# Performance work log

Measured on AMD Instinct MI355X. Metric: run time of the kernel, lower is better.

The kernel has to match this reference:

```python
import jax, jax.numpy as jnp
import numpy as np

N_NODES = 100000
N_EDGES = 1600000
IN_FEATS = 128
OUT_FEATS = 32


def setup_inputs() -> dict:
    key = jax.random.key(0)
    k1, k2, k3, k4 = jax.random.split(key, 4)
    inputs = jax.random.normal(k1, (N_NODES, IN_FEATS), dtype=jnp.float32)
    weight = jax.random.normal(k2, (IN_FEATS, OUT_FEATS), dtype=jnp.float32)
    src = jax.random.randint(k3, (N_EDGES,), 0, N_NODES, dtype=jnp.int32)
    dst = jax.random.randint(k4, (N_EDGES,), 0, N_NODES, dtype=jnp.int32)
    return {"inputs": inputs, "weight": weight, "src": src, "dst": dst}


def reference(inputs, weight, src, dst):
    # GCNLayer.forward: dense projection then sparse sum-aggregation (gspmmv,
    # no normalization: norm flags False/False -> plain neighbor sum).
    h = inputs @ weight                      # [N, out_feats]
    msgs = h[src]                            # gather over edges [E, out_feats]
    out = jax.ops.segment_sum(msgs, dst, num_segments=inputs.shape[0])
    return out
```

## Files before the change

kernel.cpp:

```cpp
#include <hip/hip_runtime.h>
#include <hip/hip_bf16.h>

#define N_F_IN 128
#define N_F_OUT 32

#define BSHIFT 7
#define BNODES 128
#define BCAP 2560
#define SCAT_EDGES 4096
#define NBL 1024
#define OFFT_LD 400

typedef __attribute__((ext_vector_type(8))) short short8v;
typedef __attribute__((ext_vector_type(4))) float float4v;

static __device__ __forceinline__ unsigned bf16pair(float a, float b) {
    unsigned ua = __float_as_uint(a), ub = __float_as_uint(b);
    ua = (ua + 0x7FFFu + ((ua >> 16) & 1u)) >> 16;
    ub = (ub + 0x7FFFu + ((ub >> 16) & 1u)) >> 16;
    return ua | (ub << 16);
}
static __device__ __forceinline__ unsigned short bf16r(float a) {
    unsigned ua = __float_as_uint(a);
    return (unsigned short)((ua + 0x7FFFu + ((ua >> 16) & 1u)) >> 16);
}

union SharedU {
    unsigned short wT[32 * 136];
    struct {
        int A[NBL];
        int B[NBL];
        int wsum[8];
        int lrec[SCAT_EDGES];
    } sc;
};

__global__ __launch_bounds__(512, 8) void fused2_kernel(const float* __restrict__ x,
                                                        const float* __restrict__ w,
                                                        unsigned short* __restrict__ hb,
                                                        int n,
                                                        const int* __restrict__ src,
                                                        const int* __restrict__ dst,
                                                        int* __restrict__ recs,
                                                        unsigned short* __restrict__ offT,
                                                        int E) {
    __shared__ SharedU u;
    const int t = threadIdx.x;
    const int nch = (E + SCAT_EDGES - 1) / SCAT_EDGES;
    const int chunk = blockIdx.x >> 1;

    if (((blockIdx.x & 1) == 0) && (chunk < nch)) {
        const int e0 = chunk * SCAT_EDGES;
        const int cnt = min(SCAT_EDGES, E - e0);

        int dv[8], sv[8];
        #pragma unroll
        for (int j = 0; j < 8; ++j) {
            int i = t + j * 512;
            dv[j] = -1; sv[j] = 0;
            if (i < cnt) { dv[j] = dst[e0 + i]; sv[j] = src[e0 + i]; }
        }

        for (int i = t; i < NBL; i += 512) u.sc.A[i] = 0;
        __syncthreads();

        #pragma unroll
        for (int j = 0; j < 8; ++j)
            if (dv[j] >= 0) atomicAdd(&u.sc.A[dv[j] >> BSHIFT], 1);
        __syncthreads();

        const int b0 = t * 2;
        const int c0 = u.sc.A[b0], c1 = u.sc.A[b0 + 1];
        const int tot = c0 + c1;
        const int lane = t & 63;
        const int wv8 = t >> 6;
        int sc = tot;
        #pragma unroll
        for (int off = 1; off < 64; off <<= 1) {
            int v = __shfl_up(sc, off, 64);
            if (lane >= off) sc += v;
        }
        if (lane == 63) u.sc.wsum[wv8] = sc;
        __syncthreads();
        int wbase = 0;
        #pragma unroll
        for (int ww = 0; ww < 7; ++ww) wbase += (ww < wv8) ? u.sc.wsum[ww] : 0;
        const int base = wbase + sc - tot;
        u.sc.B[b0] = base;
        u.sc.B[b0 + 1] = base + c0;
        offT[(long)b0 * OFFT_LD + chunk]       = (unsigned short)base;
        offT[(long)(b0 + 1) * OFFT_LD + chunk] = (unsigned short)(base + c0);
        __syncthreads();

        #pragma unroll
        for (int j = 0; j < 8; ++j) {
            if (dv[j] >= 0) {
                int r = atomicAdd(&u.sc.B[dv[j] >> BSHIFT], 1);
                u.sc.lrec[r] = ((dv[j] & (BNODES - 1)) << 17) | sv[j];
            }
        }
        __syncthreads();

        {
            int* rp = recs + (long)chunk * SCAT_EDGES;
            for (int i = t; i < cnt; i += 512) rp[i] = u.sc.lrec[i];
        }
        __syncthreads();
    }

    {
        const float4* w4 = (const float4*)w;
        float4 a = w4[t * 2], bq = w4[t * 2 + 1];
        int idx = t * 8;
        u.wT[((idx + 0) & 31) * 136 + ((idx + 0) >> 5)] = bf16r(a.x);
        u.wT[((idx + 1) & 31) * 136 + ((idx + 1) >> 5)] = bf16r(a.y);
        u.wT[((idx + 2) & 31) * 136 + ((idx + 2) >> 5)] = bf16r(a.z);
        u.wT[((idx + 3) & 31) * 136 + ((idx + 3) >> 5)] = bf16r(a.w);
        u.wT[((idx + 4) & 31) * 136 + ((idx + 4) >> 5)] = bf16r(bq.x);
        u.wT[((idx + 5) & 31) * 136 + ((idx + 5) >> 5)] = bf16r(bq.y);
        u.wT[((idx + 6) & 31) * 136 + ((idx + 6) >> 5)] = bf16r(bq.z);
        u.wT[((idx + 7) & 31) * 136 + ((idx + 7) >> 5)] = bf16r(bq.w);
    }
    __syncthreads();

    const int wv = t >> 6;
    const int l = t & 63;
    const int lr = l & 15;
    const int lg = l >> 4;

    const int ntiles = (n + 15) >> 4;
    const int mtile = blockIdx.x * 8 + wv;
    if (mtile < ntiles) {
        const long R0 = (long)mtile * 16;
        long rr = R0 + lr; if (rr >= n) rr = n - 1;
        const float4* q = (const float4*)(x + rr * N_F_IN) + lg * 2;

        const unsigned short* wr0 = &u.wT[lr * 136];
        const unsigned short* wr1 = &u.wT[(16 + lr) * 136];

        float4 p0 = q[0], p1 = q[1], p2 = q[8], p3 = q[9];
        float4v acc0 = {0.f, 0.f, 0.f, 0.f}, acc1 = {0.f, 0.f, 0.f, 0.f};
        #pragma unroll
        for (int ks = 0; ks < 4; ++ks) {
            float4 lo, hi;
            if (ks & 1) { lo = p2; hi = p3; } else { lo = p0; hi = p1; }
            union { short8v v; unsigned uu[4]; } af;
            af.uu[0] = bf16pair(lo.x, lo.y);
            af.uu[1] = bf16pair(lo.z, lo.w);
            af.uu[2] = bf16pair(hi.x, hi.y);
            af.uu[3] = bf16pair(hi.z, hi.w);
            if (ks == 0) { p0 = q[16]; p1 = q[17]; }
            if (ks == 1) { p2 = q[24]; p3 = q[25]; }
            short8v bf0 = *(const short8v*)(wr0 + ks * 32 + lg * 8);
            short8v bf1 = *(const short8v*)(wr1 + ks * 32 + lg * 8);
            acc0 = __builtin_amdgcn_mfma_f32_16x16x32_bf16(af.v, bf0, acc0, 0, 0, 0);
            acc1 = __builtin_amdgcn_mfma_f32_16x16x32_bf16(af.v, bf1, acc1, 0, 0, 0);
        }
        #pragma unroll
        for (int reg = 0; reg < 4; ++reg) {
            long row = R0 + lg * 4 + reg;
            if (row < n) {
                hb[row * N_F_OUT + lr]      = bf16r(acc0[reg]);
                hb[row * N_F_OUT + 16 + lr] = bf16r(acc1[reg]);
            }
        }
    }
}

__global__ __launch_bounds__(512) void agg_kernel(const unsigned short* __restrict__ hb,
                                                  const unsigned short* __restrict__ offT,
                                                  const int* __restrict__ recs,
                                                  float* __restrict__ out, int n, int nch) {
    __shared__ unsigned short s_st[OFFT_LD], s_en[OFFT_LD];
    __shared__ int dof[512];
    __shared__ int srt0[BCAP];
    __shared__ int srt[BCAP];
    __shared__ int cN[BNODES], loff[BNODES + 1], lc[BNODES], wsum8[8];
    __shared__ int s_tot;
    const int t = threadIdx.x;
    const int b = blockIdx.x;

    for (int i = t; i < nch; i += 512) {
        s_st[i] = offT[(long)b * OFFT_LD + i];
        s_en[i] = offT[(long)(b + 1) * OFFT_LD + i];
    }
    if (t < BNODES) cN[t] = 0;
    __syncthreads();

    const int cc = (t < nch) ? ((int)s_en[t] - (int)s_st[t]) : 0;
    const int lane = t & 63;
    const int wv = t >> 6;
    int sc = cc;
    #pragma unroll
    for (int off = 1; off < 64; off <<= 1) {
        int v = __shfl_up(sc, off, 64);
        if (lane >= off) sc += v;
    }
    if (lane == 63) wsum8[wv] = sc;
    __syncthreads();
    int wbase = 0;
    #pragma unroll
    for (int ww = 0; ww < 7; ++ww) wbase += (ww < wv) ? wsum8[ww] : 0;
    dof[t] = wbase + sc - cc;
    if (t == 511) s_tot = wbase + sc;
    __syncthreads();
    const int cnt = min(s_tot, BCAP);

    for (int i = t; i < cnt; i += 512) {
        int lo = 0, hi = nch;
        while (hi - lo > 1) {
            int mid = (lo + hi) >> 1;
            if (dof[mid] <= i) lo = mid; else hi = mid;
        }
        srt0[i] = recs[(long)lo * SCAT_EDGES + (int)s_st[lo] + (i - dof[lo])];
    }
    __syncthreads();

    int i = t;
    for (; i + 1536 < cnt; i += 2048) {
        int r0 = srt0[i],        r1 = srt0[i + 512];
        int r2 = srt0[i + 1024], r3 = srt0[i + 1536];
        atomicAdd(&cN[(r0 >> 17) & (BNODES - 1)], 1);
        atomicAdd(&cN[(r1 >> 17) & (BNODES - 1)], 1);
        atomicAdd(&cN[(r2 >> 17) & (BNODES - 1)], 1);
        atomicAdd(&cN[(r3 >> 17) & (BNODES - 1)], 1);
    }
    for (; i < cnt; i += 512)
        atomicAdd(&cN[(srt0[i] >> 17) & (BNODES - 1)], 1);
    __syncthreads();

    if (t < 64) {
        int v0 = cN[2 * t], v1 = cN[2 * t + 1];
        int s = v0 + v1;
        #pragma unroll
        for (int off = 1; off < 64; off <<= 1) {
            int v = __shfl_up(s, off, 64);
            if (t >= off) s += v;
        }
        int ex = s - v0 - v1;
        loff[2 * t] = ex;
        loff[2 * t + 1] = ex + v0;
        lc[2 * t] = ex;
        lc[2 * t + 1] = ex + v0;
        if (t == 63) loff[BNODES] = s;
    }
    __syncthreads();

    i = t;
    for (; i + 1536 < cnt; i += 2048) {
        int r0 = srt0[i],        r1 = srt0[i + 512];
        int r2 = srt0[i + 1024], r3 = srt0[i + 1536];
        int k0 = atomicAdd(&lc[(r0 >> 17) & (BNODES - 1)], 1); srt[k0] = r0 & 0x1FFFF;
        int k1 = atomicAdd(&lc[(r1 >> 17) & (BNODES - 1)], 1); srt[k1] = r1 & 0x1FFFF;
        int k2 = atomicAdd(&lc[(r2 >> 17) & (BNODES - 1)], 1); srt[k2] = r2 & 0x1FFFF;
        int k3 = atomicAdd(&lc[(r3 >> 17) & (BNODES - 1)], 1); srt[k3] = r3 & 0x1FFFF;
    }
    for (; i < cnt; i += 512) {
        int r0 = srt0[i];
        int k0 = atomicAdd(&lc[(r0 >> 17) & (BNODES - 1)], 1); srt[k0] = r0 & 0x1FFFF;
    }
    __syncthreads();

    const uint2* hq = (const uint2*)hb;
    #pragma unroll
    for (int pp = 0; pp < 2; ++pp) {
        int nl = pp * 64 + (t >> 3);
        int jj = t & 7;
        int beg = loff[nl], end = loff[nl + 1];
        float4 a0 = make_float4(0.f, 0.f, 0.f, 0.f);
        float4 a1 = a0, a2 = a0, a3 = a0;
        int k = beg;
        for (; k + 4 <= end; k += 4) {
            uint2 v0 = hq[(size_t)srt[k] * 8 + jj];
            uint2 v1 = hq[(size_t)srt[k + 1] * 8 + jj];
            uint2 v2 = hq[(size_t)srt[k + 2] * 8 + jj];
            uint2 v3 = hq[(size_t)srt[k + 3] * 8 + jj];
            a0.x += __uint_as_float(v0.x << 16); a0.y += __uint_as_float(v0.x & 0xFFFF0000u);
            a0.z += __uint_as_float(v0.y << 16); a0.w += __uint_as_float(v0.y & 0xFFFF0000u);
            a1.x += __uint_as_float(v1.x << 16); a1.y += __uint_as_float(v1.x & 0xFFFF0000u);
            a1.z += __uint_as_float(v1.y << 16); a1.w += __uint_as_float(v1.y & 0xFFFF0000u);
            a2.x += __uint_as_float(v2.x << 16); a2.y += __uint_as_float(v2.x & 0xFFFF0000u);
            a2.z += __uint_as_float(v2.y << 16); a2.w += __uint_as_float(v2.y & 0xFFFF0000u);
            a3.x += __uint_as_float(v3.x << 16); a3.y += __uint_as_float(v3.x & 0xFFFF0000u);
            a3.z += __uint_as_float(v3.y << 16); a3.w += __uint_as_float(v3.y & 0xFFFF0000u);
        }
        for (; k < end; ++k) {
            uint2 v0 = hq[(size_t)srt[k] * 8 + jj];
            a0.x += __uint_as_float(v0.x << 16); a0.y += __uint_as_float(v0.x & 0xFFFF0000u);
            a0.z += __uint_as_float(v0.y << 16); a0.w += __uint_as_float(v0.y & 0xFFFF0000u);
        }
        float4 a = make_float4(a0.x + a1.x + a2.x + a3.x, a0.y + a1.y + a2.y + a3.y,
                               a0.z + a1.z + a2.z + a3.z, a0.w + a1.w + a2.w + a3.w);
        long node = (long)b * BNODES + nl;
        if (node < n) *(float4*)&out[node * N_F_OUT + jj * 4] = a;
    }
}

extern "C" void kernel_launch(void* const* d_in, const int* in_sizes, int n_in,
                              void* d_out, int out_size, void* d_ws, size_t ws_size,
                              hipStream_t stream) {
    const float* x = (const float*)d_in[0];
    const float* w = (const float*)d_in[1];
    const int* src = (const int*)d_in[2];
    const int* dst = (const int*)d_in[3];
    float* out = (float*)d_out;

    const int n = in_sizes[0] / N_F_IN;
    const int E = in_sizes[2];
    const int NB = (n + BNODES - 1) >> BSHIFT;
    const int nch = (E + SCAT_EDGES - 1) / SCAT_EDGES;

    char* p = (char*)d_ws;
    unsigned short* hb = (unsigned short*)p;
    p += (((size_t)n * N_F_OUT * sizeof(unsigned short)) + 255) & ~(size_t)255;
    int* recs = (int*)p;
    p += (((size_t)nch * SCAT_EDGES * sizeof(int)) + 255) & ~(size_t)255;
    unsigned short* offT = (unsigned short*)p;
    p += (((size_t)1025 * OFFT_LD * sizeof(unsigned short)) + 255) & ~(size_t)255;

    const int ntiles = (n + 15) >> 4;
    int nblk = (ntiles + 7) >> 3;
    if (nblk < 2 * nch) nblk = 2 * nch;

    fused2_kernel<<<nblk, 512, 0, stream>>>(x, w, hb, n, src, dst, recs, offT, E);
    agg_kernel<<<NB, 512, 0, stream>>>(hb, offT, recs, out, n, nch);
}
```

Measured before the change: 56.58 us.

## Rebalance GEMM tiles across scatter/GEMM block pairs and replace binary search in aggregation

In the fused kernel, each block pair now shares 16 GEMM tiles: the scatter block takes 5 and the GEMM-only block takes 11, so work is balanced against the scatter cost. The weight load is hoisted ahead of the scatter phase, and the record copy-out is vectorized to int4. In the aggregation kernel, the per-element binary search over chunk offsets is replaced by a marker array plus a max prefix scan, with the bucket counting fused into the gather. The gather loop is unrolled to 8 loads with two accumulators. These changes add a few more barriers and more register pressure.

```diff
diff --git a/kernel.cpp b/kernel.cpp
--- a/kernel.cpp
+++ b/kernel.cpp
@@ -47,10 +47,14 @@
     __shared__ SharedU u;
     const int t = threadIdx.x;
     const int nch = (E + SCAT_EDGES - 1) / SCAT_EDGES;
-    const int chunk = blockIdx.x >> 1;
-
-    if (((blockIdx.x & 1) == 0) && (chunk < nch)) {
-        const int e0 = chunk * SCAT_EDGES;
+    const int pair = blockIdx.x >> 1;
+    const bool isScat = ((blockIdx.x & 1) == 0) && (pair < nch);
+
+    const float4* w4 = (const float4*)w;
+    const float4 wa = w4[t * 2], wb = w4[t * 2 + 1];
+
+    if (isScat) {
+        const int e0 = pair * SCAT_EDGES;
         const int cnt = min(SCAT_EDGES, E - e0);
 
         int dv[8], sv[8];
@@ -88,8 +92,8 @@
         const int base = wbase + sc - tot;
         u.sc.B[b0] = base;
         u.sc.B[b0 + 1] = base + c0;
-        offT[(long)b0 * OFFT_LD + chunk]       = (unsigned short)base;
-        offT[(long)(b0 + 1) * OFFT_LD + chunk] = (unsigned short)(base + c0);
+        offT[(long)b0 * OFFT_LD + pair]       = (unsigned short)base;
+        offT[(long)(b0 + 1) * OFFT_LD + pair] = (unsigned short)(base + c0);
         __syncthreads();
 
         #pragma unroll
@@ -102,41 +106,42 @@
         __syncthreads();
 
         {
-            int* rp = recs + (long)chunk * SCAT_EDGES;
-            for (int i = t; i < cnt; i += 512) rp[i] = u.sc.lrec[i];
+            int* rp = recs + (long)pair * SCAT_EDGES;
+            const int4* lr4 = (const int4*)u.sc.lrec;
+            int4* rp4 = (int4*)rp;
+            const int c4 = cnt >> 2;
+            for (int i = t; i < c4; i += 512) rp4[i] = lr4[i];
+            for (int i = (c4 << 2) + t; i < cnt; i += 512) rp[i] = u.sc.lrec[i];
         }
         __syncthreads();
     }
 
     {
-        const float4* w4 = (const float4*)w;
-        float4 a = w4[t * 2], bq = w4[t * 2 + 1];
         int idx = t * 8;
-        u.wT[((idx + 0) & 31) * 136 + ((idx + 0) >> 5)] = bf16r(a.x);
-        u.wT[((idx + 1) & 31) * 136 + ((idx + 1) >> 5)] = bf16r(a.y);
-        u.wT[((idx + 2) & 31) * 136 + ((idx + 2) >> 5)] = bf16r(a.z);
-        u.wT[((idx + 3) & 31) * 136 + ((idx + 3) >> 5)] = bf16r(a.w);
-        u.wT[((idx + 4) & 31) * 136 + ((idx + 4) >> 5)] = bf16r(bq.x);
-        u.wT[((idx + 5) & 31) * 136 + ((idx + 5) >> 5)] = bf16r(bq.y);
-        u.wT[((idx + 6) & 31) * 136 + ((idx + 6) >> 5)] = bf16r(bq.z);
-        u.wT[((idx + 7) & 31) * 136 + ((idx + 7) >> 5)] = bf16r(bq.w);
-    }
-    __syncthreads();
-
-    const int wv = t >> 6;
+        u.wT[((idx + 0) & 31) * 136 + ((idx + 0) >> 5)] = bf16r(wa.x);
+        u.wT[((idx + 1) & 31) * 136 + ((idx + 1) >> 5)] = bf16r(wa.y);
+        u.wT[((idx + 2) & 31) * 136 + ((idx + 2) >> 5)] = bf16r(wa.z);
+        u.wT[((idx + 3) & 31) * 136 + ((idx + 3) >> 5)] = bf16r(wa.w);
+        u.wT[((idx + 4) & 31) * 136 + ((idx + 4) >> 5)] = bf16r(wb.x);
+        u.wT[((idx + 5) & 31) * 136 + ((idx + 5) >> 5)] = bf16r(wb.y);
+        u.wT[((idx + 6) & 31) * 136 + ((idx + 6) >> 5)] = bf16r(wb.z);
+        u.wT[((idx + 7) & 31) * 136 + ((idx + 7) >> 5)] = bf16r(wb.w);
+    }
+    __syncthreads();
+
+    const int wvid = t >> 6;
     const int l = t & 63;
     const int lr = l & 15;
     const int lg = l >> 4;
-
     const int ntiles = (n + 15) >> 4;
-    const int mtile = blockIdx.x * 8 + wv;
-    if (mtile < ntiles) {
+
+    const unsigned short* wr0 = &u.wT[lr * 136];
+    const unsigned short* wr1 = &u.wT[(16 + lr) * 136];
+
+    auto gemm_tile = [&](int mtile) {
         const long R0 = (long)mtile * 16;
         long rr = R0 + lr; if (rr >= n) rr = n - 1;
         const float4* q = (const float4*)(x + rr * N_F_IN) + lg * 2;
-
-        const unsigned short* wr0 = &u.wT[lr * 136];
-        const unsigned short* wr1 = &u.wT[(16 + lr) * 136];
 
         float4 p0 = q[0], p1 = q[1], p2 = q[8], p3 = q[9];
         float4v acc0 = {0.f, 0.f, 0.f, 0.f}, acc1 = {0.f, 0.f, 0.f, 0.f};
@@ -164,6 +169,17 @@
                 hb[row * N_F_OUT + 16 + lr] = bf16r(acc1[reg]);
             }
         }
+    };
+
+    const int tbase = pair * 16;
+    if (blockIdx.x & 1) {
+        int m0 = tbase + 5 + wvid;
+        if (m0 < ntiles) gemm_tile(m0);
+        int m1 = tbase + 13 + wvid;
+        if (wvid < 3 && m1 < ntiles) gemm_tile(m1);
+    } else {
+        int m0 = tbase + wvid;
+        if (wvid < 5 && m0 < ntiles) gemm_tile(m0);
     }
 }
 
@@ -171,25 +187,23 @@
                                                   const unsigned short* __restrict__ offT,
                                                   const int* __restrict__ recs,
                                                   float* __restrict__ out, int n, int nch) {
-    __shared__ unsigned short s_st[OFFT_LD], s_en[OFFT_LD];
+    __shared__ unsigned short s_st[OFFT_LD];
     __shared__ int dof[512];
     __shared__ int srt0[BCAP];
-    __shared__ int srt[BCAP];
+    __shared__ int chk_srt[BCAP];
     __shared__ int cN[BNODES], loff[BNODES + 1], lc[BNODES], wsum8[8];
     __shared__ int s_tot;
     const int t = threadIdx.x;
     const int b = blockIdx.x;
-
-    for (int i = t; i < nch; i += 512) {
-        s_st[i] = offT[(long)b * OFFT_LD + i];
-        s_en[i] = offT[(long)(b + 1) * OFFT_LD + i];
-    }
-    if (t < BNODES) cN[t] = 0;
-    __syncthreads();
-
-    const int cc = (t < nch) ? ((int)s_en[t] - (int)s_st[t]) : 0;
     const int lane = t & 63;
     const int wv = t >> 6;
+
+    for (int i = t; i < nch; i += 512) s_st[i] = offT[(long)b * OFFT_LD + i];
+    int en_t = (t < nch) ? (int)offT[(long)(b + 1) * OFFT_LD + t] : 0;
+    if (t < BNODES) cN[t] = 0;
+    __syncthreads();
+
+    const int cc = (t < nch) ? (en_t - (int)s_st[t]) : 0;
     int sc = cc;
     #pragma unroll
     for (int off = 1; off < 64; off <<= 1) {
@@ -201,32 +215,57 @@
     int wbase = 0;
     #pragma unroll
     for (int ww = 0; ww < 7; ++ww) wbase += (ww < wv) ? wsum8[ww] : 0;
-    dof[t] = wbase + sc - cc;
+    const int mydof = wbase + sc - cc;
+    dof[t] = mydof;
     if (t == 511) s_tot = wbase + sc;
     __syncthreads();
     const int cnt = min(s_tot, BCAP);
 
-    for (int i = t; i < cnt; i += 512) {
-        int lo = 0, hi = nch;
-        while (hi - lo > 1) {
-            int mid = (lo + hi) >> 1;
-            if (dof[mid] <= i) lo = mid; else hi = mid;
-        }
-        srt0[i] = recs[(long)lo * SCAT_EDGES + (int)s_st[lo] + (i - dof[lo])];
-    }
-    __syncthreads();
-
-    int i = t;
-    for (; i + 1536 < cnt; i += 2048) {
-        int r0 = srt0[i],        r1 = srt0[i + 512];
-        int r2 = srt0[i + 1024], r3 = srt0[i + 1536];
-        atomicAdd(&cN[(r0 >> 17) & (BNODES - 1)], 1);
-        atomicAdd(&cN[(r1 >> 17) & (BNODES - 1)], 1);
-        atomicAdd(&cN[(r2 >> 17) & (BNODES - 1)], 1);
-        atomicAdd(&cN[(r3 >> 17) & (BNODES - 1)], 1);
-    }
-    for (; i < cnt; i += 512)
-        atomicAdd(&cN[(srt0[i] >> 17) & (BNODES - 1)], 1);
+    for (int i = t; i < cnt; i += 512) chk_srt[i] = 0;
+    __syncthreads();
+    if (t < nch && cc > 0) chk_srt[mydof] = t;
+    __syncthreads();
+
+    int m0 = 0, m1 = 0, m2 = 0, m3 = 0, m4 = 0;
+    {
+        int i0 = t * 5;
+        if (i0 + 0 < cnt) m0 = chk_srt[i0 + 0];
+        if (i0 + 1 < cnt) m1 = chk_srt[i0 + 1];
+        if (i0 + 2 < cnt) m2 = chk_srt[i0 + 2];
+        if (i0 + 3 < cnt) m3 = chk_srt[i0 + 3];
+        if (i0 + 4 < cnt) m4 = chk_srt[i0 + 4];
+    }
+    int sm0 = m0, sm1 = max(sm0, m1), sm2 = max(sm1, m2), sm3 = max(sm2, m3), sm4 = max(sm3, m4);
+    int tmax = sm4;
+    #pragma unroll
+    for (int off = 1; off < 64; off <<= 1) {
+        int v = __shfl_up(tmax, off, 64);
+        if (lane >= off) tmax = max(tmax, v);
+    }
+    if (lane == 63) wsum8[wv] = tmax;
+    int excl = __shfl_up(tmax, 1, 64);
+    if (lane == 0) excl = 0;
+    __syncthreads();
+    int wmax = 0;
+    #pragma unroll
+    for (int ww = 0; ww < 7; ++ww) wmax = (ww < wv) ? max(wmax, wsum8[ww]) : wmax;
+    const int p = max(wmax, excl);
+
+    {
+        int i0 = t * 5;
+        int r0 = max(p, sm0), r1 = max(p, sm1), r2 = max(p, sm2), r3 = max(p, sm3), r4 = max(p, sm4);
+        int v0 = 0, v1 = 0, v2 = 0, v3 = 0, v4 = 0;
+        if (i0 + 0 < cnt) v0 = recs[(long)r0 * SCAT_EDGES + (int)s_st[r0] + (i0 + 0 - dof[r0])];
+        if (i0 + 1 < cnt) v1 = recs[(long)r1 * SCAT_EDGES + (int)s_st[r1] + (i0 + 1 - dof[r1])];
+        if (i0 + 2 < cnt) v2 = recs[(long)r2 * SCAT_EDGES + (int)s_st[r2] + (i0 + 2 - dof[r2])];
+        if (i0 + 3 < cnt) v3 = recs[(long)r3 * SCAT_EDGES + (int)s_st[r3] + (i0 + 3 - dof[r3])];
+        if (i0 + 4 < cnt) v4 = recs[(long)r4 * SCAT_EDGES + (int)s_st[r4] + (i0 + 4 - dof[r4])];
+        if (i0 + 0 < cnt) { srt0[i0 + 0] = v0; atomicAdd(&cN[(v0 >> 17) & (BNODES - 1)], 1); }
+        if (i0 + 1 < cnt) { srt0[i0 + 1] = v1; atomicAdd(&cN[(v1 >> 17) & (BNODES - 1)], 1); }
+        if (i0 + 2 < cnt) { srt0[i0 + 2] = v2; atomicAdd(&cN[(v2 >> 17) & (BNODES - 1)], 1); }
+        if (i0 + 3 < cnt) { srt0[i0 + 3] = v3; atomicAdd(&cN[(v3 >> 17) & (BNODES - 1)], 1); }
+        if (i0 + 4 < cnt) { srt0[i0 + 4] = v4; atomicAdd(&cN[(v4 >> 17) & (BNODES - 1)], 1); }
+    }
     __syncthreads();
 
     if (t < 64) {
@@ -246,18 +285,18 @@
     }
     __syncthreads();
 
-    i = t;
+    int i = t;
     for (; i + 1536 < cnt; i += 2048) {
         int r0 = srt0[i],        r1 = srt0[i + 512];
         int r2 = srt0[i + 1024], r3 = srt0[i + 1536];
-        int k0 = atomicAdd(&lc[(r0 >> 17) & (BNODES - 1)], 1); srt[k0] = r0 & 0x1FFFF;
-        int k1 = atomicAdd(&lc[(r1 >> 17) & (BNODES - 1)], 1); srt[k1] = r1 & 0x1FFFF;
-        int k2 = atomicAdd(&lc[(r2 >> 17) & (BNODES - 1)], 1); srt[k2] = r2 & 0x1FFFF;
-        int k3 = atomicAdd(&lc[(r3 >> 17) & (BNODES - 1)], 1); srt[k3] = r3 & 0x1FFFF;
+        int k0 = atomicAdd(&lc[(r0 >> 17) & (BNODES - 1)], 1); chk_srt[k0] = r0 & 0x1FFFF;
+        int k1 = atomicAdd(&lc[(r1 >> 17) & (BNODES - 1)], 1); chk_srt[k1] = r1 & 0x1FFFF;
+        int k2 = atomicAdd(&lc[(r2 >> 17) & (BNODES - 1)], 1); chk_srt[k2] = r2 & 0x1FFFF;
+        int k3 = atomicAdd(&lc[(r3 >> 17) & (BNODES - 1)], 1); chk_srt[k3] = r3 & 0x1FFFF;
     }
     for (; i < cnt; i += 512) {
         int r0 = srt0[i];
-        int k0 = atomicAdd(&lc[(r0 >> 17) & (BNODES - 1)], 1); srt[k0] = r0 & 0x1FFFF;
+        int k0 = atomicAdd(&lc[(r0 >> 17) & (BNODES - 1)], 1); chk_srt[k0] = r0 & 0x1FFFF;
     }
     __syncthreads();
 
@@ -268,29 +307,54 @@
         int jj = t & 7;
         int beg = loff[nl], end = loff[nl + 1];
         float4 a0 = make_float4(0.f, 0.f, 0.f, 0.f);
-        float4 a1 = a0, a2 = a0, a3 = a0;
+        float4 a1 = a0;
         int k = beg;
-        for (; k + 4 <= end; k += 4) {
-            uint2 v0 = hq[(size_t)srt[k] * 8 + jj];
-            uint2 v1 = hq[(size_t)srt[k + 1] * 8 + jj];
-            uint2 v2 = hq[(size_t)srt[k + 2] * 8 + jj];
-            uint2 v3 = hq[(size_t)srt[k + 3] * 8 + jj];
+        for (; k + 8 <= end; k += 8) {
+            uint2 v0 = hq[(size_t)chk_srt[k] * 8 + jj];
+            uint2 v1 = hq[(size_t)chk_srt[k + 1] * 8 + jj];
+            uint2 v2 = hq[(size_t)chk_srt[k + 2] * 8 + jj];
+            uint2 v3 = hq[(size_t)chk_srt[k + 3] * 8 + jj];
+            uint2 v4 = hq[(size_t)chk_srt[k + 4] * 8 + jj];
+            uint2 v5 = hq[(size_t)chk_srt[k + 5] * 8 + jj];
+            uint2 v6 = hq[(size_t)chk_srt[k + 6] * 8 + jj];
+            uint2 v7 = hq[(size_t)chk_srt[k + 7] * 8 + jj];
             a0.x += __uint_as_float(v0.x << 16); a0.y += __uint_as_float(v0.x & 0xFFFF0000u);
             a0.z += __uint_as_float(v0.y << 16); a0.w += __uint_as_float(v0.y & 0xFFFF0000u);
             a1.x += __uint_as_float(v1.x << 16); a1.y += __uint_as_float(v1.x & 0xFFFF0000u);
             a1.z += __uint_as_float(v1.y << 16); a1.w += __uint_as_float(v1.y & 0xFFFF0000u);
-            a2.x += __uint_as_float(v2.x << 16); a2.y += __uint_as_float(v2.x & 0xFFFF0000u);
-            a2.z += __uint_as_float(v2.y << 16); a2.w += __uint_as_float(v2.y & 0xFFFF0000u);
-            a3.x += __uint_as_float(v3.x << 16); a3.y += __uint_as_float(v3.x & 0xFFFF0000u);
-            a3.z += __uint_as_float(v3.y << 16); a3.w += __uint_as_float(v3.y & 0xFFFF0000u);
-        }
-        for (; k < end; ++k) {
-            uint2 v0 = hq[(size_t)srt[k] * 8 + jj];
+            a0.x += __uint_as_float(v2.x << 16); a0.y += __uint_as_float(v2.x & 0xFFFF0000u);
+            a0.z += __uint_as_float(v2.y << 16); a0.w += __uint_as_float(v2.y & 0xFFFF0000u);
+            a1.x += __uint_as_float(v3.x << 16); a1.y += __uint_as_float(v3.x & 0xFFFF0000u);
+            a1.z += __uint_as_float(v3.y << 16); a1.w += __uint_as_float(v3.y & 0xFFFF0000u);
+            a0.x += __uint_as_float(v4.x << 16); a0.y += __uint_as_float(v4.x & 0xFFFF0000u);
+            a0.z += __uint_as_float(v4.y << 16); a0.w += __uint_as_float(v4.y & 0xFFFF0000u);
+            a1.x += __uint_as_float(v5.x << 16); a1.y += __uint_as_float(v5.x & 0xFFFF0000u);
+            a1.z += __uint_as_float(v5.y << 16); a1.w += __uint_as_float(v5.y & 0xFFFF0000u);
+            a0.x += __uint_as_float(v6.x << 16); a0.y += __uint_as_float(v6.x & 0xFFFF0000u);
+            a0.z += __uint_as_float(v6.y << 16); a0.w += __uint_as_float(v6.y & 0xFFFF0000u);
+            a1.x += __uint_as_float(v7.x << 16); a1.y += __uint_as_float(v7.x & 0xFFFF0000u);
+            a1.z += __uint_as_float(v7.y << 16); a1.w += __uint_as_float(v7.y & 0xFFFF0000u);
+        }
+        for (; k + 4 <= end; k += 4) {
+            uint2 v0 = hq[(size_t)chk_srt[k] * 8 + jj];
+            uint2 v1 = hq[(size_t)chk_srt[k + 1] * 8 + jj];
+            uint2 v2 = hq[(size_t)chk_srt[k + 2] * 8 + jj];
+            uint2 v3 = hq[(size_t)chk_srt[k + 3] * 8 + jj];
             a0.x += __uint_as_float(v0.x << 16); a0.y += __uint_as_float(v0.x & 0xFFFF0000u);
             a0.z += __uint_as_float(v0.y << 16); a0.w += __uint_as_float(v0.y & 0xFFFF0000u);
-        }
-        float4 a = make_float4(a0.x + a1.x + a2.x + a3.x, a0.y + a1.y + a2.y + a3.y,
-                               a0.z + a1.z + a2.z + a3.z, a0.w + a1.w + a2.w + a3.w);
+            a1.x += __uint_as_float(v1.x << 16); a1.y += __uint_as_float(v1.x & 0xFFFF0000u);
+            a1.z += __uint_as_float(v1.y << 16); a1.w += __uint_as_float(v1.y & 0xFFFF0000u);
+            a0.x += __uint_as_float(v2.x << 16); a0.y += __uint_as_float(v2.x & 0xFFFF0000u);
+            a0.z += __uint_as_float(v2.y << 16); a0.w += __uint_as_float(v2.y & 0xFFFF0000u);
+            a1.x += __uint_as_float(v3.x << 16); a1.y += __uint_as_float(v3.x & 0xFFFF0000u);
+            a1.z += __uint_as_float(v3.y << 16); a1.w += __uint_as_float(v3.y & 0xFFFF0000u);
+        }
+        for (; k < end; ++k) {
+            uint2 v0 = hq[(size_t)chk_srt[k] * 8 + jj];
+            a0.x += __uint_as_float(v0.x << 16); a0.y += __uint_as_float(v0.x & 0xFFFF0000u);
+            a0.z += __uint_as_float(v0.y << 16); a0.w += __uint_as_float(v0.y & 0xFFFF0000u);
+        }
+        float4 a = make_float4(a0.x + a1.x, a0.y + a1.y, a0.z + a1.z, a0.w + a1.w);
         long node = (long)b * BNODES + nl;
         if (node < n) *(float4*)&out[node * N_F_OUT + jj * 4] = a;
     }
@@ -319,8 +383,9 @@
     p += (((size_t)1025 * OFFT_LD * sizeof(unsigned short)) + 255) & ~(size_t)255;
 
     const int ntiles = (n + 15) >> 4;
-    int nblk = (ntiles + 7) >> 3;
-    if (nblk < 2 * nch) nblk = 2 * nch;
+    const int npair_t = (ntiles + 15) >> 4;
+    int npair = (nch > npair_t) ? nch : npair_t;
+    const int nblk = 2 * npair;
 
     fused2_kernel<<<nblk, 512, 0, stream>>>(x, w, hb, n, src, dst, recs, offT, E);
     agg_kernel<<<NB, 512, 0, stream>>>(hb, offT, recs, out, n, nch);
```

After: 58.51 us. 3.4% more time.
